# Performance work log

Hardware: AMD Instinct MI355X
Metric: run time of the kernel (lower is better)

Reference implementation:

```python
import jax, jax.numpy as jnp
import numpy as np

N_QUBITS = 6
BLOCKS = 3
LATENT = 3
DIM = 1 << N_QUBITS  # 64, state-vector size
BATCH = 131072
INP_DIM = 6  # must equal N_QUBITS (repo applies linear_pre to the n_qubits-dim recon)

# Wire 0 is the most-significant qubit (PennyLane convention).
_idx = np.arange(DIM)
BITS = ((_idx[:, None] >> (N_QUBITS - 1 - np.arange(N_QUBITS))) & 1)  # (64, 6)
# Chain of CZ(k, k+1): all diagonal, fold into one sign vector per block.
CZ_SIGN = jnp.asarray(np.prod(1 - 2 * (BITS[:, :-1] * BITS[:, 1:]), axis=1).astype(np.float32))  # (64,)
Z_SIGNS = jnp.asarray((1 - 2 * BITS).astype(np.float32))  # (64, 6): <Z_k> signs per basis state


def _apply_1q(state, U, wire):
    # state: (B, 64) complex64; U: (2,2) complex64 acting on `wire`
    B = state.shape[0]
    s = state.reshape(B, 1 << wire, 2, 1 << (N_QUBITS - 1 - wire))
    s = jnp.einsum('ij,bxjy->bxiy', U, s)
    return s.reshape(B, DIM)


def _circuit(amps, weights, n_out):
    # AmplitudeEmbedding with normalize=True (x was already unit-normed in torch; idempotent)
    norm = jnp.linalg.norm(amps, axis=1, keepdims=True)
    state = (amps / norm).astype(jnp.complex64)  # (B, 64)
    for j in range(BLOCKS):
        for k in range(N_QUBITS):
            tx = weights[j, k, 0]
            tz = weights[j, k, 1]
            c = jnp.cos(0.5 * tx).astype(jnp.complex64)
            s = jnp.sin(0.5 * tx).astype(jnp.complex64)
            em = jnp.exp(-0.5j * tz).astype(jnp.complex64)
            ep = jnp.exp(0.5j * tz).astype(jnp.complex64)
            # Fused U = RZ(tz) @ RX(tx)
            U = jnp.stack([jnp.stack([em * c, -1j * em * s]),
                           jnp.stack([-1j * ep * s, ep * c])])
            state = _apply_1q(state, U, k)
        state = state * CZ_SIGN  # all CZ gates of the block, fused
    probs = state.real ** 2 + state.imag ** 2  # (B, 64)
    return probs @ Z_SIGNS[:, :n_out]  # expval(PauliZ(k)) for k < n_out


def setup_inputs() -> dict:
    key = jax.random.key(0)
    k1, k2, k3, k4, k5 = jax.random.split(key, 5)
    x = jax.random.normal(k1, (BATCH, INP_DIM), dtype=jnp.float32)
    bound = 1.0 / np.sqrt(INP_DIM)
    W_pre = jax.random.uniform(k2, (DIM, INP_DIM), minval=-bound, maxval=bound, dtype=jnp.float32)
    b_pre = jax.random.uniform(k3, (DIM,), minval=-bound, maxval=bound, dtype=jnp.float32)
    enc_w = jax.random.normal(k4, (BLOCKS, N_QUBITS, 3), dtype=jnp.float32) * 0.01
    dec_w = jax.random.normal(k5, (BLOCKS, N_QUBITS, 3), dtype=jnp.float32) * 0.01
    return {'x': x, 'W_pre': W_pre, 'b_pre': b_pre, 'enc_w': enc_w, 'dec_w': dec_w}


def reference(x, W_pre, b_pre, enc_w, dec_w):
    h = jnp.tanh(x @ W_pre.T + b_pre)                     # (B, 64)
    latent = _circuit(h, enc_w, LATENT)                    # (B, 3)
    padded = jnp.zeros((x.shape[0], DIM), jnp.float32).at[:, :LATENT].set(latent)
    recon = _circuit(padded, dec_w, N_QUBITS)              # (B, 6)
    reconstructed = jnp.tanh(recon @ W_pre.T + b_pre)      # (B, 64)
    return reconstructed, latent
```

## Files before the change

### kernel.cpp

```cpp
#include <hip/hip_runtime.h>

#define BATCH 131072

typedef float v2f __attribute__((ext_vector_type(2)));


__device__ __forceinline__ float fast_tanh(float v) {
    float e = __expf(2.0f * v);
    return 1.0f - 2.0f / (e + 1.0f);
}

template <int CTRL>
__device__ __forceinline__ float dppf(float v) {
    return __int_as_float(__builtin_amdgcn_update_dpp(
        0, __float_as_int(v), CTRL, 0xF, 0xF, true));
}
#define DPP_XOR1 0xB1
#define DPP_XOR2 0x4E

__device__ __forceinline__ v2f swap2(v2f v) { return __builtin_shufflevector(v, v, 1, 0); }

__global__ __launch_bounds__(256) void prep_kernel(const float* __restrict__ enc_w,
                                                   const float* __restrict__ dec_w,
                                                   float* __restrict__ ws) {
    __shared__ float gt[18][8];
    __shared__ float Sr[64][8];
    __shared__ float Si[64][8];
    const int t = threadIdx.x;

    if (t < 18) {
        float tx = dec_w[t * 3 + 0];
        float tz = dec_w[t * 3 + 1];
        float c = cosf(0.5f * tx), s = sinf(0.5f * tx);
        float ch = cosf(0.5f * tz), sh = sinf(0.5f * tz);
        gt[t][0] = c * ch;  gt[t][1] = -c * sh;
        gt[t][2] = -s * sh; gt[t][3] = -s * ch;
        gt[t][4] = s * sh;  gt[t][5] = -s * ch;
        gt[t][6] = c * ch;  gt[t][7] = c * sh;
    }

    const int cl = t & 7;
    const int pr = t >> 3;
    float* fSr = &Sr[0][0];
    float* fSi = &Si[0][0];
    for (int f = t; f < 512; f += 256) {
        int r = f >> 3, c = f & 7;
        fSr[f] = (r == c && c < 3) ? 1.0f : 0.0f;
        fSi[f] = 0.0f;
    }

    for (int bb = 0; bb < 3; ++bb) {
        for (int w = 0; w < 6; ++w) {
            __syncthreads();
            int g = bb * 6 + w;
            int p = 5 - w;
            float u00r = gt[g][0], u00i = gt[g][1], u01r = gt[g][2], u01i = gt[g][3];
            float u10r = gt[g][4], u10i = gt[g][5], u11r = gt[g][6], u11i = gt[g][7];
            int r0 = ((pr >> p) << (p + 1)) | (pr & ((1 << p) - 1));
            int r1 = r0 | (1 << p);
            float ar = Sr[r0][cl], ai = Si[r0][cl];
            float br = Sr[r1][cl], bi = Si[r1][cl];
            Sr[r0][cl] = u00r * ar - u00i * ai + u01r * br - u01i * bi;
            Si[r0][cl] = u00r * ai + u00i * ar + u01r * bi + u01i * br;
            Sr[r1][cl] = u10r * ar - u10i * ai + u11r * br - u11i * bi;
            Si[r1][cl] = u10r * ai + u10i * ar + u11r * bi + u11i * br;
        }
        __syncthreads();
        for (int f = t; f < 512; f += 256) {
            int r = f >> 3;
            if (__popc(r & (r >> 1)) & 1) {
                fSr[f] = -fSr[f];
                fSi[f] = -fSi[f];
            }
        }
    }
    __syncthreads();

    if (t < 54) {
        int k = t / 9, d = (t % 9) / 3, e = t % 3;
        float acc = 0.0f;
        for (int r = 0; r < 64; ++r) {
            float term = Sr[r][d] * Sr[r][e] + Si[r][d] * Si[r][e];
            acc += ((r >> (5 - k)) & 1) ? -term : term;
        }
        ws[t] = acc;
    }

    if (t < 18) {
        float tx = enc_w[t * 3 + 0];
        ws[64 + 2 * t] = cosf(0.5f * tx);
        ws[65 + 2 * t] = sinf(0.5f * tx);
    }

    if (t >= 64 && t < 256) {
        int idx = t - 64;
        int bb = idx >> 6, r = idx & 63;
        float phi = 0.0f;
        for (int k = 0; k < 6; ++k) {
            float tz = enc_w[(bb * 6 + k) * 3 + 1];
            phi += ((r >> (5 - k)) & 1) ? 0.5f * tz : -0.5f * tz;
        }
        float sgn = (__popc(r & (r >> 1)) & 1) ? -1.0f : 1.0f;
        ws[128 + bb * 128 + 2 * r] = sgn * cosf(phi);
        ws[129 + bb * 128 + 2 * r] = sgn * sinf(phi);
    }
}

template <int MASK>
__device__ __forceinline__ void rx_pairs(v2f* zr, v2f* zi, float c, float s) {
#pragma unroll
    for (int j = 0; j < 8; ++j) {
        if (j & MASK) continue;
        int j1 = j | MASK;
        v2f ar = zr[j], ai = zi[j], br = zr[j1], bi = zi[j1];
        zr[j]  = c * ar + s * bi;
        zi[j]  = c * ai - s * br;
        zr[j1] = c * br + s * ai;
        zi[j1] = c * bi - s * ar;
    }
}

template <int CTRL>
__device__ __forceinline__ void rx_exch2(v2f* zr, v2f* zi, float c, float s) {
#pragma unroll
    for (int j = 0; j < 8; ++j) {
        v2f pr, pi;
        pr.x = dppf<CTRL>(zr[j].x);
        pr.y = dppf<CTRL>(zr[j].y);
        pi.x = dppf<CTRL>(zi[j].x);
        pi.y = dppf<CTRL>(zi[j].y);
        v2f mr = zr[j], mi = zi[j];
        zr[j] = c * mr + s * pi;
        zi[j] = c * mi - s * pr;
    }
}

__global__ __launch_bounds__(256) void qae_main(const float* __restrict__ x,
                                                const float* __restrict__ Wp,
                                                const float* __restrict__ bp,
                                                const float* __restrict__ ws,
                                                float* __restrict__ out) {
    __shared__ float sW[540];
    __shared__ float sD[256];
    __shared__ float sLat[192];

    const int t = threadIdx.x;
    const int bl = t >> 2;
    const int sub = t & 3;

    for (int f = t; f < 512; f += 256) {
        int g = f >> 4, e = f & 15;
        int j = g >> 2, su = g & 3;
        float val;
        if (e < 12)      { int row = 8 * j + su + 4 * (e & 1); val = Wp[row * 6 + (e >> 1)]; }
        else if (e < 14) { int row = 8 * j + su + 4 * (e - 12); val = bp[row]; }
        else val = 0.0f;
        sW[g * 16 + j * 4 + e] = val;
    }
    if (t < 128) {
        int bb = t >> 6, r = t & 63;
        int su = r & 3, m = r >> 2, j = m >> 1, hm = m & 1;
        int base = ((bb * 8 + j) * 4 + su) * 4;
        sD[base + hm]     = ws[128 + bb * 128 + 2 * r];
        sD[base + 2 + hm] = ws[128 + bb * 128 + 2 * r + 1];
    }
    __syncthreads();

    const size_t b = (size_t)blockIdx.x * 64 + bl;
    const float* xp = x + b * 6;
    float2 x01 = *(const float2*)(xp);
    float2 x23 = *(const float2*)(xp + 2);
    float2 x45 = *(const float2*)(xp + 4);
    float xv[6] = {x01.x, x01.y, x23.x, x23.y, x45.x, x45.y};

    v2f zr[8], zi[8];
    v2f S2 = {0.0f, 0.0f};
#pragma unroll
    for (int j = 0; j < 8; ++j) {
        const float* wb = &sW[(j * 4 + sub) * 16 + j * 4];
        float4 c0 = *(const float4*)wb;
        float4 c1 = *(const float4*)(wb + 4);
        float4 c2 = *(const float4*)(wb + 8);
        float4 c3 = *(const float4*)(wb + 12);
        v2f a = {c3.x, c3.y};
        a += xv[0] * (v2f){c0.x, c0.y};
        a += xv[1] * (v2f){c0.z, c0.w};
        a += xv[2] * (v2f){c1.x, c1.y};
        a += xv[3] * (v2f){c1.z, c1.w};
        a += xv[4] * (v2f){c2.x, c2.y};
        a += xv[5] * (v2f){c2.z, c2.w};
        v2f th = {fast_tanh(a.x), fast_tanh(a.y)};
        zr[j] = th;
        zi[j] = (v2f){0.0f, 0.0f};
        S2 += th * th;
    }
    float S = S2.x + S2.y;
    S += dppf<DPP_XOR1>(S);
    S += dppf<DPP_XOR2>(S);
    float invS = __builtin_amdgcn_rcpf(S);

#pragma unroll 1
    for (int bb = 0; bb < 3; ++bb) {
        const float* rx = ws + 64 + 12 * bb;
        rx_pairs<4>(zr, zi, rx[0], rx[1]);
        rx_pairs<2>(zr, zi, rx[2], rx[3]);
        rx_pairs<1>(zr, zi, rx[4], rx[5]);
        {
            float c = rx[6], s = rx[7];
#pragma unroll
            for (int j = 0; j < 8; ++j) {
                v2f orr = zr[j], oi = zi[j];
                zr[j] = c * orr + s * swap2(oi);
                zi[j] = c * oi - s * swap2(orr);
            }
        }
        rx_exch2<DPP_XOR2>(zr, zi, rx[8], rx[9]);
        rx_exch2<DPP_XOR1>(zr, zi, rx[10], rx[11]);
        if (bb < 2) {
#pragma unroll
            for (int j = 0; j < 8; ++j) {
                float4 d = *(const float4*)&sD[((bb * 8 + j) * 4 + sub) * 4];
                v2f dr = {d.x, d.y}, di = {d.z, d.w};
                v2f orr = zr[j], oi = zi[j];
                zr[j] = dr * orr - di * oi;
                zi[j] = dr * oi + di * orr;
            }
        }
    }

    v2f L0 = {0, 0}, L1 = {0, 0}, L2 = {0, 0};
#pragma unroll
    for (int j = 0; j < 8; ++j) {
        v2f p = zr[j] * zr[j] + zi[j] * zi[j];
        L0 += (j & 4) ? -p : p;
        L1 += (j & 2) ? -p : p;
        L2 += (j & 1) ? -p : p;
    }
    float l0 = L0.x + L0.y, l1 = L1.x + L1.y, l2 = L2.x + L2.y;
    l0 += dppf<DPP_XOR1>(l0); l0 += dppf<DPP_XOR2>(l0);
    l1 += dppf<DPP_XOR1>(l1); l1 += dppf<DPP_XOR2>(l1);
    l2 += dppf<DPP_XOR1>(l2); l2 += dppf<DPP_XOR2>(l2);
    l0 *= invS; l1 *= invS; l2 *= invS;

    float r2 = l0 * l0 + l1 * l1 + l2 * l2;
    float invr2 = __builtin_amdgcn_rcpf(r2);
    float lv[3] = {l0, l1, l2};
    float rec[6];
#pragma unroll
    for (int k = 0; k < 6; ++k) {
        float acc = 0.0f;
#pragma unroll
        for (int d = 0; d < 3; ++d)
#pragma unroll
            for (int e = 0; e < 3; ++e) acc += ws[k * 9 + d * 3 + e] * lv[d] * lv[e];
        rec[k] = acc * invr2;
    }

    if (sub == 0) {
        sLat[bl * 3 + 0] = l0;
        sLat[bl * 3 + 1] = l1;
        sLat[bl * 3 + 2] = l2;
    }
    __syncthreads();
    if (t < 192) out[(size_t)BATCH * 64 + (size_t)blockIdx.x * 192 + t] = sLat[t];

    const size_t ob = b * 64;
#pragma unroll
    for (int jj = 0; jj < 2; ++jj) {
        int jrow = 2 * sub + jj;
        float vlo[4], vhi[4];
#pragma unroll
        for (int su2 = 0; su2 < 4; ++su2) {
            int g = jrow * 4 + su2;
            const float* wb = &sW[g * 16 + jrow * 4];
            float4 c0 = *(const float4*)wb;
            float4 c1 = *(const float4*)(wb + 4);
            float4 c2 = *(const float4*)(wb + 8);
            float2 b2 = *(const float2*)(wb + 12);
            v2f a = {b2.x, b2.y};
            a += rec[0] * (v2f){c0.x, c0.y};
            a += rec[1] * (v2f){c0.z, c0.w};
            a += rec[2] * (v2f){c1.x, c1.y};
            a += rec[3] * (v2f){c1.z, c1.w};
            a += rec[4] * (v2f){c2.x, c2.y};
            a += rec[5] * (v2f){c2.z, c2.w};
            vlo[su2] = fast_tanh(a.x);
            vhi[su2] = fast_tanh(a.y);
        }
        float4 o0 = {vlo[0], vlo[1], vlo[2], vlo[3]};
        float4 o1 = {vhi[0], vhi[1], vhi[2], vhi[3]};
        *(float4*)&out[ob + 8 * jrow]     = o0;
        *(float4*)&out[ob + 8 * jrow + 4] = o1;
    }
}

extern "C" void kernel_launch(void* const* d_in, const int* in_sizes, int n_in,
                              void* d_out, int out_size, void* d_ws, size_t ws_size,
                              hipStream_t stream) {
    const float* x   = (const float*)d_in[0];
    const float* Wp  = (const float*)d_in[1];
    const float* bpv = (const float*)d_in[2];
    const float* enc = (const float*)d_in[3];
    const float* dec = (const float*)d_in[4];
    float* out = (float*)d_out;
    float* ws  = (float*)d_ws;

    prep_kernel<<<1, 256, 0, stream>>>(enc, dec, ws);
    qae_main<<<(BATCH * 4) / 256, 256, 0, stream>>>(x, Wp, bpv, ws, out);
}
```

Measured before the change: 105.4 us.

## Use packed f32 inline asm for gate math and unroll encoder blocks

Replaces the vector-typed complex arithmetic in the encoder gates, the linear layers and the probability sum with explicit v_pk_mul_f32 and v_pk_fma_f32 inline asm, using op_sel and neg modifiers to fold swaps and negations into the packed instructions. The three encoder blocks are now fully unrolled through a templated function, and the first RX gate uses a cheaper real-only form because the state has no imaginary part yet. Gate coefficients are preloaded into registers rather than read from global memory inside the loop. This aims to halve VALU instruction count on the compute-bound circuit simulation, at the cost of higher register pressure and opaque asm that limits compiler scheduling.

Result: no change. 106.1 us (+0.6%).

```diff
diff --git a/kernel.cpp b/kernel.cpp
--- a/kernel.cpp
+++ b/kernel.cpp
@@ -18,7 +18,27 @@
 #define DPP_XOR1 0xB1
 #define DPP_XOR2 0x4E
 
-__device__ __forceinline__ v2f swap2(v2f v) { return __builtin_shufflevector(v, v, 1, 0); }
+__device__ __forceinline__ v2f pk_mul(v2f a, v2f b) {
+    v2f d; asm("v_pk_mul_f32 %0, %1, %2" : "=v"(d) : "v"(a), "v"(b)); return d;
+}
+__device__ __forceinline__ v2f pk_fma(v2f a, v2f b, v2f c) {
+    v2f d; asm("v_pk_fma_f32 %0, %1, %2, %3" : "=v"(d) : "v"(a), "v"(b), "v"(c)); return d;
+}
+__device__ __forceinline__ v2f pk_fma_n0(v2f a, v2f b, v2f c) {
+    v2f d; asm("v_pk_fma_f32 %0, %1, %2, %3 neg_lo:[1,0,0] neg_hi:[1,0,0]"
+               : "=v"(d) : "v"(a), "v"(b), "v"(c)); return d;
+}
+__device__ __forceinline__ v2f pk_fma_sw0(v2f a, v2f b, v2f c) {
+    v2f d; asm("v_pk_fma_f32 %0, %1, %2, %3 op_sel:[1,0,0] op_sel_hi:[0,1,1]"
+               : "=v"(d) : "v"(a), "v"(b), "v"(c)); return d;
+}
+__device__ __forceinline__ v2f pk_fma_sw0n(v2f a, v2f b, v2f c) {
+    v2f d; asm("v_pk_fma_f32 %0, %1, %2, %3 op_sel:[1,0,0] op_sel_hi:[0,1,1] neg_lo:[1,0,0] neg_hi:[1,0,0]"
+               : "=v"(d) : "v"(a), "v"(b), "v"(c)); return d;
+}
+__device__ __forceinline__ v2f tanh2(v2f a) {
+    return (v2f){fast_tanh(a.x), fast_tanh(a.y)};
+}
 
 __global__ __launch_bounds__(256) void prep_kernel(const float* __restrict__ enc_w,
                                                    const float* __restrict__ dec_w,
@@ -107,21 +127,48 @@
 }
 
 template <int MASK>
-__device__ __forceinline__ void rx_pairs(v2f* zr, v2f* zi, float c, float s) {
+__device__ __forceinline__ void rx_pk(v2f* zr, v2f* zi, float c, float s) {
+    v2f cc = {c, c}, ss = {s, s};
 #pragma unroll
     for (int j = 0; j < 8; ++j) {
         if (j & MASK) continue;
         int j1 = j | MASK;
         v2f ar = zr[j], ai = zi[j], br = zr[j1], bi = zi[j1];
-        zr[j]  = c * ar + s * bi;
-        zi[j]  = c * ai - s * br;
-        zr[j1] = c * br + s * ai;
-        zi[j1] = c * bi - s * ar;
+        zr[j]  = pk_fma(ss, bi, pk_mul(cc, ar));
+        zi[j]  = pk_fma_n0(ss, br, pk_mul(cc, ai));
+        zr[j1] = pk_fma(ss, ai, pk_mul(cc, br));
+        zi[j1] = pk_fma_n0(ss, ar, pk_mul(cc, bi));
+    }
+}
+
+template <int MASK>
+__device__ __forceinline__ void rx_pk_real(v2f* zr, v2f* zi, float c, float s) {
+    v2f cc = {c, c}, sn = {-s, -s};
+#pragma unroll
+    for (int j = 0; j < 8; ++j) {
+        if (j & MASK) continue;
+        int j1 = j | MASK;
+        v2f ar = zr[j], br = zr[j1];
+        zr[j]  = pk_mul(cc, ar);
+        zi[j]  = pk_mul(sn, br);
+        zr[j1] = pk_mul(cc, br);
+        zi[j1] = pk_mul(sn, ar);
+    }
+}
+
+__device__ __forceinline__ void rx_inpack(v2f* zr, v2f* zi, float c, float s) {
+    v2f cc = {c, c}, ss = {s, s};
+#pragma unroll
+    for (int j = 0; j < 8; ++j) {
+        v2f orr = zr[j], oi = zi[j];
+        zr[j] = pk_fma_sw0(oi, ss, pk_mul(cc, orr));
+        zi[j] = pk_fma_sw0n(orr, ss, pk_mul(cc, oi));
     }
 }
 
 template <int CTRL>
-__device__ __forceinline__ void rx_exch2(v2f* zr, v2f* zi, float c, float s) {
+__device__ __forceinline__ void rx_dpp(v2f* zr, v2f* zi, float c, float s) {
+    v2f cc = {c, c}, ss = {s, s};
 #pragma unroll
     for (int j = 0; j < 8; ++j) {
         v2f pr, pi;
@@ -130,8 +177,30 @@
         pi.x = dppf<CTRL>(zi[j].x);
         pi.y = dppf<CTRL>(zi[j].y);
         v2f mr = zr[j], mi = zi[j];
-        zr[j] = c * mr + s * pi;
-        zi[j] = c * mi - s * pr;
+        zr[j] = pk_fma(ss, pi, pk_mul(cc, mr));
+        zi[j] = pk_fma_n0(ss, pr, pk_mul(cc, mi));
+    }
+}
+
+template <int BB>
+__device__ __forceinline__ void enc_block(v2f* zr, v2f* zi, const float* rxc,
+                                          const float* sD, int sub) {
+    if (BB == 0) rx_pk_real<4>(zr, zi, rxc[12 * BB + 0], rxc[12 * BB + 1]);
+    else         rx_pk<4>(zr, zi, rxc[12 * BB + 0], rxc[12 * BB + 1]);
+    rx_pk<2>(zr, zi, rxc[12 * BB + 2], rxc[12 * BB + 3]);
+    rx_pk<1>(zr, zi, rxc[12 * BB + 4], rxc[12 * BB + 5]);
+    rx_inpack(zr, zi, rxc[12 * BB + 6], rxc[12 * BB + 7]);
+    rx_dpp<DPP_XOR2>(zr, zi, rxc[12 * BB + 8], rxc[12 * BB + 9]);
+    rx_dpp<DPP_XOR1>(zr, zi, rxc[12 * BB + 10], rxc[12 * BB + 11]);
+    if (BB < 2) {
+#pragma unroll
+        for (int j = 0; j < 8; ++j) {
+            float4 d = *(const float4*)&sD[((BB * 8 + j) * 4 + sub) * 4];
+            v2f dr = {d.x, d.y}, di = {d.z, d.w};
+            v2f orr = zr[j], oi = zi[j];
+            zr[j] = pk_fma_n0(di, oi, pk_mul(dr, orr));
+            zi[j] = pk_fma(di, orr, pk_mul(dr, oi));
+        }
     }
 }
 
@@ -164,6 +233,10 @@
         sD[base + hm]     = ws[128 + bb * 128 + 2 * r];
         sD[base + 2 + hm] = ws[128 + bb * 128 + 2 * r + 1];
     }
+
+    float rxc[36];
+#pragma unroll
+    for (int i = 0; i < 36; ++i) rxc[i] = ws[64 + i];
     __syncthreads();
 
     const size_t b = (size_t)blockIdx.x * 64 + bl;
@@ -171,7 +244,10 @@
     float2 x01 = *(const float2*)(xp);
     float2 x23 = *(const float2*)(xp + 2);
     float2 x45 = *(const float2*)(xp + 4);
-    float xv[6] = {x01.x, x01.y, x23.x, x23.y, x45.x, x45.y};
+    v2f xq[6];
+    xq[0] = (v2f){x01.x, x01.x}; xq[1] = (v2f){x01.y, x01.y};
+    xq[2] = (v2f){x23.x, x23.x}; xq[3] = (v2f){x23.y, x23.y};
+    xq[4] = (v2f){x45.x, x45.x}; xq[5] = (v2f){x45.y, x45.y};
 
     v2f zr[8], zi[8];
     v2f S2 = {0.0f, 0.0f};
@@ -183,55 +259,30 @@
         float4 c2 = *(const float4*)(wb + 8);
         float4 c3 = *(const float4*)(wb + 12);
         v2f a = {c3.x, c3.y};
-        a += xv[0] * (v2f){c0.x, c0.y};
-        a += xv[1] * (v2f){c0.z, c0.w};
-        a += xv[2] * (v2f){c1.x, c1.y};
-        a += xv[3] * (v2f){c1.z, c1.w};
-        a += xv[4] * (v2f){c2.x, c2.y};
-        a += xv[5] * (v2f){c2.z, c2.w};
-        v2f th = {fast_tanh(a.x), fast_tanh(a.y)};
+        a = pk_fma(xq[0], (v2f){c0.x, c0.y}, a);
+        a = pk_fma(xq[1], (v2f){c0.z, c0.w}, a);
+        a = pk_fma(xq[2], (v2f){c1.x, c1.y}, a);
+        a = pk_fma(xq[3], (v2f){c1.z, c1.w}, a);
+        a = pk_fma(xq[4], (v2f){c2.x, c2.y}, a);
+        a = pk_fma(xq[5], (v2f){c2.z, c2.w}, a);
+        v2f th = tanh2(a);
         zr[j] = th;
         zi[j] = (v2f){0.0f, 0.0f};
-        S2 += th * th;
+        S2 = pk_fma(th, th, S2);
     }
     float S = S2.x + S2.y;
     S += dppf<DPP_XOR1>(S);
     S += dppf<DPP_XOR2>(S);
     float invS = __builtin_amdgcn_rcpf(S);
 
-#pragma unroll 1
-    for (int bb = 0; bb < 3; ++bb) {
-        const float* rx = ws + 64 + 12 * bb;
-        rx_pairs<4>(zr, zi, rx[0], rx[1]);
-        rx_pairs<2>(zr, zi, rx[2], rx[3]);
-        rx_pairs<1>(zr, zi, rx[4], rx[5]);
-        {
-            float c = rx[6], s = rx[7];
-#pragma unroll
-            for (int j = 0; j < 8; ++j) {
-                v2f orr = zr[j], oi = zi[j];
-                zr[j] = c * orr + s * swap2(oi);
-                zi[j] = c * oi - s * swap2(orr);
-            }
-        }
-        rx_exch2<DPP_XOR2>(zr, zi, rx[8], rx[9]);
-        rx_exch2<DPP_XOR1>(zr, zi, rx[10], rx[11]);
-        if (bb < 2) {
-#pragma unroll
-            for (int j = 0; j < 8; ++j) {
-                float4 d = *(const float4*)&sD[((bb * 8 + j) * 4 + sub) * 4];
-                v2f dr = {d.x, d.y}, di = {d.z, d.w};
-                v2f orr = zr[j], oi = zi[j];
-                zr[j] = dr * orr - di * oi;
-                zi[j] = dr * oi + di * orr;
-            }
-        }
-    }
+    enc_block<0>(zr, zi, rxc, sD, sub);
+    enc_block<1>(zr, zi, rxc, sD, sub);
+    enc_block<2>(zr, zi, rxc, sD, sub);
 
     v2f L0 = {0, 0}, L1 = {0, 0}, L2 = {0, 0};
 #pragma unroll
     for (int j = 0; j < 8; ++j) {
-        v2f p = zr[j] * zr[j] + zi[j] * zi[j];
+        v2f p = pk_fma(zi[j], zi[j], pk_mul(zr[j], zr[j]));
         L0 += (j & 4) ? -p : p;
         L1 += (j & 2) ? -p : p;
         L2 += (j & 1) ? -p : p;
@@ -252,7 +303,7 @@
 #pragma unroll
         for (int d = 0; d < 3; ++d)
 #pragma unroll
-            for (int e = 0; e < 3; ++e) acc += ws[k * 9 + d * 3 + e] * lv[d] * lv[e];
+            for (int e2 = 0; e2 < 3; ++e2) acc += ws[k * 9 + d * 3 + e2] * lv[d] * lv[e2];
         rec[k] = acc * invr2;
     }
 
@@ -264,6 +315,9 @@
     __syncthreads();
     if (t < 192) out[(size_t)BATCH * 64 + (size_t)blockIdx.x * 192 + t] = sLat[t];
 
+    v2f rq[6];
+#pragma unroll
+    for (int d = 0; d < 6; ++d) rq[d] = (v2f){rec[d], rec[d]};
     const size_t ob = b * 64;
 #pragma unroll
     for (int jj = 0; jj < 2; ++jj) {
@@ -278,12 +332,12 @@
             float4 c2 = *(const float4*)(wb + 8);
             float2 b2 = *(const float2*)(wb + 12);
             v2f a = {b2.x, b2.y};
-            a += rec[0] * (v2f){c0.x, c0.y};
-            a += rec[1] * (v2f){c0.z, c0.w};
-            a += rec[2] * (v2f){c1.x, c1.y};
-            a += rec[3] * (v2f){c1.z, c1.w};
-            a += rec[4] * (v2f){c2.x, c2.y};
-            a += rec[5] * (v2f){c2.z, c2.w};
+            a = pk_fma(rq[0], (v2f){c0.x, c0.y}, a);
+            a = pk_fma(rq[1], (v2f){c0.z, c0.w}, a);
+            a = pk_fma(rq[2], (v2f){c1.x, c1.y}, a);
+            a = pk_fma(rq[3], (v2f){c1.z, c1.w}, a);
+            a = pk_fma(rq[4], (v2f){c2.x, c2.y}, a);
+            a = pk_fma(rq[5], (v2f){c2.z, c2.w}, a);
             vlo[su2] = fast_tanh(a.x);
             vhi[su2] = fast_tanh(a.y);
         }
```
